# Performance work log

Hardware: AMD Instinct MI355X
Metric: run time of the kernel (lower is better)

## Reference

```python
import jax, jax.numpy as jnp
import numpy as np

B, N, C, O, S = 32, 256, 512, 512, 512  # batch, table_num, in_ch, out_ch, s_dim


def setup_inputs() -> dict:
    key = jax.random.key(0)
    k1, k2, k3, k4 = jax.random.split(key, 4)
    # xavier_normal on (N, O, C): fan_in = O*C? torch treats dim0 fan_out, dim1 fan_in, rest receptive
    fan_out, fan_in = N * C, O * C
    std = float(np.sqrt(2.0 / (fan_in + fan_out)))
    weight = jax.random.normal(k1, (N, O, C), dtype=jnp.float32) * std
    bias = jnp.zeros((1, N, O), dtype=jnp.float32)
    # StyleGAN FullyConnectedLayer(s_dim -> table_num, bias_init=1): raw randn weight,
    # weight_gain = 1/sqrt(s_dim) applied at forward, bias init to 1
    s_w = jax.random.normal(k2, (N, S), dtype=jnp.float32)
    s_b = jnp.ones((N,), dtype=jnp.float32)
    x = jax.random.normal(k3, (B, N, C), dtype=jnp.float32)
    s = jax.random.normal(k4, (B, S), dtype=jnp.float32)
    return {"x": x, "s": s, "weight": weight, "bias": bias, "s_w": s_w, "s_b": s_b}


def reference(x, s, weight, bias, s_w, s_b):
    # style mapping: FullyConnectedLayer with weight_gain = 1/sqrt(s_dim)
    gain = 1.0 / np.sqrt(S)
    s_map = s @ (s_w.T * gain) + s_b  # (B, N)
    # demodulation: rsqrt(sum_c (weight*s)^2 + eps) == rsqrt(s^2 * sum_c weight^2 + eps)
    sumsq = jnp.sum(weight * weight, axis=-1)  # (N, O)
    decoefs = jax.lax.rsqrt(s_map[:, :, None] ** 2 * sumsq[None] + 1e-8)  # (B, N, O)
    xs = x * s_map[:, :, None]  # (B, N, C)
    out = jnp.einsum('noc,bnc->bno', weight, xs)  # (B, N, O)
    out = out * decoefs + bias
    return out
```

## Files before the change

kernel.cpp:

```cpp
#include <hip/hip_runtime.h>

#define B_ 32
#define N_ 256
#define C_ 512
#define O_ 512
#define S_ 512

#define KT  64
#define NKT (C_ / KT)
#define WST 72

typedef __attribute__((ext_vector_type(8))) short short8;
typedef __attribute__((ext_vector_type(4))) float f32x4;

__device__ __forceinline__ short f2bf(float f) {
    union { float f; unsigned u; } v; v.f = f;
    unsigned r = v.u + 0x7fffu + ((v.u >> 16) & 1u);
    return (short)(r >> 16);
}
__device__ __forceinline__ float bf2f(short s) {
    union { unsigned u; float f; } v; v.u = ((unsigned)(unsigned short)s) << 16;
    return v.f;
}

__global__ __launch_bounds__(256, 2) void tml_kernel(const float* __restrict__ x,
                                                     const float* __restrict__ s,
                                                     const float* __restrict__ weight,
                                                     const float* __restrict__ bias,
                                                     const float* __restrict__ s_w,
                                                     const float* __restrict__ s_b,
                                                     float* __restrict__ out) {
    const int h       = blockIdx.x;
    const int logical = (h & 7) * 128 + (h >> 3);
    const int n       = logical >> 2;
    const int ot      = logical & 3;

    const int tid  = threadIdx.x;
    const int wv   = tid >> 6;
    const int lane = tid & 63;
    const int l16  = lane & 15;
    const int lk   = lane >> 4;

    __shared__ short xs[B_][C_ + 8];
    __shared__ short wt[2][128][WST];
    __shared__ float sm_lds[B_];

    const int srow = tid >> 4;
    const int scol = tid & 15;
    const float* wbase = weight + (size_t)n * (O_ * C_) + (size_t)(ot * 128) * C_ + scol * 4;

    float4 rg0[8], rg1[8];
#pragma unroll
    for (int i = 0; i < 8; ++i)
        rg0[i] = *(const float4*)(wbase + (size_t)(i * 16 + srow) * C_);

    {
        const int b    = tid >> 3;
        const int slot = tid & 7;
        const float* sp = s   + (size_t)b * S_ + slot * 64;
        const float* wp = s_w + (size_t)n * S_ + slot * 64;
        float sum = 0.f;
#pragma unroll
        for (int j = 0; j < 16; ++j) {
            float4 sv  = *(const float4*)(sp + 4 * j);
            float4 wv4 = *(const float4*)(wp + 4 * j);
            sum += sv.x * wv4.x + sv.y * wv4.y + sv.z * wv4.z + sv.w * wv4.w;
        }
        sum += __shfl_xor(sum, 1, 64);
        sum += __shfl_xor(sum, 2, 64);
        sum += __shfl_xor(sum, 4, 64);
        if (slot == 0) sm_lds[b] = sum * 0.04419417382415922f + s_b[n];
    }

    const float* xn = x + (size_t)n * C_;
#pragma unroll
    for (int r = 0; r < 16; ++r) {
        int i  = r * 256 + tid;
        int b  = i >> 7;
        int c4 = (i & 127) << 2;
        const float4 v = *(const float4*)(xn + (size_t)b * (N_ * C_) + c4);
        short4 hh;
        hh.x = f2bf(v.x); hh.y = f2bf(v.y); hh.z = f2bf(v.z); hh.w = f2bf(v.w);
        *(short4*)&xs[b][c4] = hh;
    }

    f32x4 acc00 = {0.f,0.f,0.f,0.f}, acc01 = acc00, acc10 = acc00, acc11 = acc00;
    float ssq0 = 0.f, ssq1 = 0.f;

#define STEP(T, RCUR, RNXT, PB)                                                   \
    {                                                                             \
        if ((T) + 1 < NKT) {                                                      \
            _Pragma("unroll")                                                     \
            for (int i = 0; i < 8; ++i)                                           \
                RNXT[i] = *(const float4*)(wbase + (size_t)(i * 16 + srow) * C_   \
                                           + ((T) + 1) * KT);                     \
        }                                                                         \
        _Pragma("unroll")                                                         \
        for (int i = 0; i < 8; ++i) {                                             \
            short4 hv;                                                            \
            hv.x = f2bf(RCUR[i].x); hv.y = f2bf(RCUR[i].y);                       \
            hv.z = f2bf(RCUR[i].z); hv.w = f2bf(RCUR[i].w);                       \
            *(short4*)&wt[PB][i * 16 + srow][scol * 4] = hv;                      \
        }                                                                         \
        __syncthreads();                                                          \
        _Pragma("unroll")                                                         \
        for (int ks = 0; ks < KT / 32; ++ks) {                                    \
            const int co = ks * 32 + lk * 8;                                      \
            short8 a0 = *(const short8*)&xs[l16][(T) * KT + co];                  \
            short8 a1 = *(const short8*)&xs[16 + l16][(T) * KT + co];             \
            short8 b0 = *(const short8*)&wt[PB][wv * 32 + l16][co];               \
            short8 b1 = *(const short8*)&wt[PB][wv * 32 + 16 + l16][co];          \
            _Pragma("unroll")                                                     \
            for (int j = 0; j < 8; ++j) {                                         \
                float f0 = bf2f(b0[j]), f1 = bf2f(b1[j]);                         \
                ssq0 += f0 * f0; ssq1 += f1 * f1;                                 \
            }                                                                     \
            acc00 = __builtin_amdgcn_mfma_f32_16x16x32_bf16(a0, b0, acc00, 0,0,0);\
            acc10 = __builtin_amdgcn_mfma_f32_16x16x32_bf16(a1, b0, acc10, 0,0,0);\
            acc01 = __builtin_amdgcn_mfma_f32_16x16x32_bf16(a0, b1, acc01, 0,0,0);\
            acc11 = __builtin_amdgcn_mfma_f32_16x16x32_bf16(a1, b1, acc11, 0,0,0);\
        }                                                                         \
    }

    STEP(0, rg0, rg1, 0)
    STEP(1, rg1, rg0, 1)
    STEP(2, rg0, rg1, 0)
    STEP(3, rg1, rg0, 1)
    STEP(4, rg0, rg1, 0)
    STEP(5, rg1, rg0, 1)
    STEP(6, rg0, rg1, 0)
    STEP(7, rg1, rg0, 1)
#undef STEP

    ssq0 += __shfl_xor(ssq0, 16, 64);  ssq0 += __shfl_xor(ssq0, 32, 64);
    ssq1 += __shfl_xor(ssq1, 16, 64);  ssq1 += __shfl_xor(ssq1, 32, 64);

    const int ob = ot * 128 + wv * 32;
#pragma unroll
    for (int f = 0; f < 2; ++f) {
        const int o  = ob + f * 16 + l16;
        const float bv = bias[n * O_ + o];
        const float sq = f ? ssq1 : ssq0;
        const f32x4 am0 = f ? acc01 : acc00;
        const f32x4 am1 = f ? acc11 : acc10;
#pragma unroll
        for (int r = 0; r < 4; ++r) {
            {
                const int brow = lk * 4 + r;
                const float smv = sm_lds[brow];
                const float dec = rsqrtf(smv * smv * sq + 1e-8f);
                out[(size_t)brow * (N_ * O_) + n * O_ + o] = am0[r] * smv * dec + bv;
            }
            {
                const int brow = 16 + lk * 4 + r;
                const float smv = sm_lds[brow];
                const float dec = rsqrtf(smv * smv * sq + 1e-8f);
                out[(size_t)brow * (N_ * O_) + n * O_ + o] = am1[r] * smv * dec + bv;
            }
        }
    }
}

extern "C" void kernel_launch(void* const* d_in, const int* in_sizes, int n_in,
                              void* d_out, int out_size, void* d_ws, size_t ws_size,
                              hipStream_t stream) {
    const float* x      = (const float*)d_in[0];
    const float* s      = (const float*)d_in[1];
    const float* weight = (const float*)d_in[2];
    const float* bias   = (const float*)d_in[3];
    const float* s_w    = (const float*)d_in[4];
    const float* s_b    = (const float*)d_in[5];
    float* out = (float*)d_out;

    tml_kernel<<<N_ * 4, 256, 0, stream>>>(x, s, weight, bias, s_w, s_b, out);
}
```

Before: 63.16 us.

## Prefetch weights two tiles ahead and compute sum-of-squares in fp32 at staging

Weight tiles are now prefetched two K-steps ahead through a three-register rotation instead of one. The demodulation sum of squares moves out of the MFMA inner loop: it is accumulated in fp32 on the staged registers, reduced with shuffles and passed to the epilogue through shared memory. The manual bf16 rounding is replaced by the packed __float22bfloat162_rn conversion. The deeper prefetch raises register pressure under the two-blocks-per-CU launch bound, and the sum of squares now uses unrounded fp32 weights rather than bf16 values.

```diff
diff --git a/kernel.cpp b/kernel.cpp
--- a/kernel.cpp
+++ b/kernel.cpp
@@ -1,4 +1,5 @@
 #include <hip/hip_runtime.h>
+#include <hip/hip_bf16.h>
 
 #define B_ 32
 #define N_ 256
@@ -7,20 +8,15 @@
 #define S_ 512
 
 #define KT  64
-#define NKT (C_ / KT)
 #define WST 72
 
 typedef __attribute__((ext_vector_type(8))) short short8;
 typedef __attribute__((ext_vector_type(4))) float f32x4;
 
-__device__ __forceinline__ short f2bf(float f) {
-    union { float f; unsigned u; } v; v.f = f;
-    unsigned r = v.u + 0x7fffu + ((v.u >> 16) & 1u);
-    return (short)(r >> 16);
-}
-__device__ __forceinline__ float bf2f(short s) {
-    union { unsigned u; float f; } v; v.u = ((unsigned)(unsigned short)s) << 16;
-    return v.f;
+__device__ __forceinline__ unsigned pk2(float a, float b) {
+    union { __hip_bfloat162 h; unsigned u; } v;
+    v.h = __float22bfloat162_rn(make_float2(a, b));
+    return v.u;
 }
 
 __global__ __launch_bounds__(256, 2) void tml_kernel(const float* __restrict__ x,
@@ -40,19 +36,23 @@
     const int lane = tid & 63;
     const int l16  = lane & 15;
     const int lk   = lane >> 4;
+    const int srow = tid >> 4;
+    const int scol = tid & 15;
 
     __shared__ short xs[B_][C_ + 8];
     __shared__ short wt[2][128][WST];
+    __shared__ float ssq_lds[128];
     __shared__ float sm_lds[B_];
 
-    const int srow = tid >> 4;
-    const int scol = tid & 15;
     const float* wbase = weight + (size_t)n * (O_ * C_) + (size_t)(ot * 128) * C_ + scol * 4;
 
-    float4 rg0[8], rg1[8];
+    float4 rgA[8], rgB[8], rgC[8];
 #pragma unroll
     for (int i = 0; i < 8; ++i)
-        rg0[i] = *(const float4*)(wbase + (size_t)(i * 16 + srow) * C_);
+        rgA[i] = *(const float4*)(wbase + (size_t)(i * 16 + srow) * C_);
+#pragma unroll
+    for (int i = 0; i < 8; ++i)
+        rgB[i] = *(const float4*)(wbase + (size_t)(i * 16 + srow) * C_ + KT);
 
     {
         const int b    = tid >> 3;
@@ -79,42 +79,49 @@
         int b  = i >> 7;
         int c4 = (i & 127) << 2;
         const float4 v = *(const float4*)(xn + (size_t)b * (N_ * C_) + c4);
-        short4 hh;
-        hh.x = f2bf(v.x); hh.y = f2bf(v.y); hh.z = f2bf(v.z); hh.w = f2bf(v.w);
-        *(short4*)&xs[b][c4] = hh;
+        *(uint2*)&xs[b][c4] = make_uint2(pk2(v.x, v.y), pk2(v.z, v.w));
     }
 
+    float ssqr[8];
+#pragma unroll
+    for (int i = 0; i < 8; ++i) ssqr[i] = 0.f;
+
     f32x4 acc00 = {0.f,0.f,0.f,0.f}, acc01 = acc00, acc10 = acc00, acc11 = acc00;
-    float ssq0 = 0.f, ssq1 = 0.f;
 
-#define STEP(T, RCUR, RNXT, PB)                                                   \
+#define STEP(T, RC, RN, PB)                                                       \
     {                                                                             \
-        if ((T) + 1 < NKT) {                                                      \
+        if ((T) + 2 < 8) {                                                        \
             _Pragma("unroll")                                                     \
             for (int i = 0; i < 8; ++i)                                           \
-                RNXT[i] = *(const float4*)(wbase + (size_t)(i * 16 + srow) * C_   \
-                                           + ((T) + 1) * KT);                     \
+                RN[i] = *(const float4*)(wbase + (size_t)(i * 16 + srow) * C_     \
+                                         + ((T) + 2) * KT);                       \
         }                                                                         \
         _Pragma("unroll")                                                         \
         for (int i = 0; i < 8; ++i) {                                             \
-            short4 hv;                                                            \
-            hv.x = f2bf(RCUR[i].x); hv.y = f2bf(RCUR[i].y);                       \
-            hv.z = f2bf(RCUR[i].z); hv.w = f2bf(RCUR[i].w);                       \
-            *(short4*)&wt[PB][i * 16 + srow][scol * 4] = hv;                      \
+            ssqr[i] += RC[i].x * RC[i].x + RC[i].y * RC[i].y                      \
+                     + RC[i].z * RC[i].z + RC[i].w * RC[i].w;                     \
+            *(uint2*)&wt[PB][i * 16 + srow][scol * 4] =                           \
+                make_uint2(pk2(RC[i].x, RC[i].y), pk2(RC[i].z, RC[i].w));         \
+        }                                                                         \
+        if ((T) == 7) {                                                           \
+            _Pragma("unroll")                                                     \
+            for (int i = 0; i < 8; ++i) {                                         \
+                float v = ssqr[i];                                                \
+                v += __shfl_xor(v, 1, 64);                                        \
+                v += __shfl_xor(v, 2, 64);                                        \
+                v += __shfl_xor(v, 4, 64);                                        \
+                v += __shfl_xor(v, 8, 64);                                        \
+                if (scol == 0) ssq_lds[i * 16 + srow] = v;                        \
+            }                                                                     \
         }                                                                         \
         __syncthreads();                                                          \
         _Pragma("unroll")                                                         \
-        for (int ks = 0; ks < KT / 32; ++ks) {                                    \
+        for (int ks = 0; ks < 2; ++ks) {                                          \
             const int co = ks * 32 + lk * 8;                                      \
             short8 a0 = *(const short8*)&xs[l16][(T) * KT + co];                  \
             short8 a1 = *(const short8*)&xs[16 + l16][(T) * KT + co];             \
             short8 b0 = *(const short8*)&wt[PB][wv * 32 + l16][co];               \
             short8 b1 = *(const short8*)&wt[PB][wv * 32 + 16 + l16][co];          \
-            _Pragma("unroll")                                                     \
-            for (int j = 0; j < 8; ++j) {                                         \
-                float f0 = bf2f(b0[j]), f1 = bf2f(b1[j]);                         \
-                ssq0 += f0 * f0; ssq1 += f1 * f1;                                 \
-            }                                                                     \
             acc00 = __builtin_amdgcn_mfma_f32_16x16x32_bf16(a0, b0, acc00, 0,0,0);\
             acc10 = __builtin_amdgcn_mfma_f32_16x16x32_bf16(a1, b0, acc10, 0,0,0);\
             acc01 = __builtin_amdgcn_mfma_f32_16x16x32_bf16(a0, b1, acc01, 0,0,0);\
@@ -122,25 +129,22 @@
         }                                                                         \
     }
 
-    STEP(0, rg0, rg1, 0)
-    STEP(1, rg1, rg0, 1)
-    STEP(2, rg0, rg1, 0)
-    STEP(3, rg1, rg0, 1)
-    STEP(4, rg0, rg1, 0)
-    STEP(5, rg1, rg0, 1)
-    STEP(6, rg0, rg1, 0)
-    STEP(7, rg1, rg0, 1)
+    STEP(0, rgA, rgC, 0)
+    STEP(1, rgB, rgA, 1)
+    STEP(2, rgC, rgB, 0)
+    STEP(3, rgA, rgC, 1)
+    STEP(4, rgB, rgA, 0)
+    STEP(5, rgC, rgB, 1)
+    STEP(6, rgA, rgC, 0)
+    STEP(7, rgB, rgC, 1)
 #undef STEP
 
-    ssq0 += __shfl_xor(ssq0, 16, 64);  ssq0 += __shfl_xor(ssq0, 32, 64);
-    ssq1 += __shfl_xor(ssq1, 16, 64);  ssq1 += __shfl_xor(ssq1, 32, 64);
-
-    const int ob = ot * 128 + wv * 32;
 #pragma unroll
     for (int f = 0; f < 2; ++f) {
-        const int o  = ob + f * 16 + l16;
+        const int orow = wv * 32 + f * 16 + l16;
+        const int o    = ot * 128 + orow;
         const float bv = bias[n * O_ + o];
-        const float sq = f ? ssq1 : ssq0;
+        const float sq = ssq_lds[orow];
         const f32x4 am0 = f ? acc01 : acc00;
         const f32x4 am1 = f ? acc11 : acc10;
 #pragma unroll
```

New measurement: 90.17 us. 42.8% more time.
